# Kernel optimization log

Measured on AMD Instinct MI355X. Metric: run time of the kernel, lower is better.

Reference implementation:

```python
import jax, jax.numpy as jnp
import numpy as np

NEIGH = 0.4  # neighborhood_size from the module


def setup_inputs() -> dict:
    key = jax.random.key(0)
    ks = jax.random.split(key, 14)
    N, E, H, G, M = 1024, 64, 128, 8, 20
    OUT = 6 * M
    f32 = jnp.float32
    inp = {
        "xabs": jax.random.uniform(ks[0], (N, 2), f32),
        "i_h0": jax.random.normal(ks[1], (1, N, H), f32) * 0.1,
        "i_c0": jax.random.normal(ks[2], (1, N, H), f32) * 0.1,
        # I_Embedding: Linear(2, E)
        "W_emb": jax.random.normal(ks[3], (E, 2), f32) * 0.5,
        "b_emb": jax.random.normal(ks[4], (E,), f32) * 0.1,
        # embedding_social: Linear(G*G*H, E)
        "W_soc": jax.random.normal(ks[5], (E, G * G * H), f32) * (1.0 / np.sqrt(G * G * H)),
        "b_soc": jax.random.normal(ks[6], (E,), f32) * 0.1,
        # LSTM(2E -> H), torch gate order [i, f, g, o]
        "W_ih": jax.random.normal(ks[7], (4 * H, 2 * E), f32) * (1.0 / np.sqrt(2 * E)),
        "W_hh": jax.random.normal(ks[8], (4 * H, H), f32) * (1.0 / np.sqrt(H)),
        "b_ih": jax.random.normal(ks[9], (4 * H,), f32) * 0.05,
        "b_hh": jax.random.normal(ks[10], (4 * H,), f32) * 0.05,
        # I_Output: Linear(H, 6*M)
        "W_out": jax.random.normal(ks[11], (OUT, H), f32) * (1.0 / np.sqrt(H)),
        "b_out": jax.random.normal(ks[12], (OUT,), f32) * 0.05,
    }
    return inp


def _grid_mask(xabs, G):
    # Vectorized getGridMask: [N, N, G*G] one-hot bin membership.
    N = xabs.shape[0]
    # dx[n, m] = other_x - width_low(n); in-range iff 0 <= dx < NEIGH
    dx = xabs[None, :, 0] - (xabs[:, None, 0] - NEIGH / 2)
    dy = xabs[None, :, 1] - (xabs[:, None, 1] - NEIGH / 2)
    cell_x = jnp.floor(dx / NEIGH * G).astype(jnp.int32)
    cell_y = jnp.floor(dy / NEIGH * G).astype(jnp.int32)
    valid = (dx >= 0) & (dx < NEIGH) & (dy >= 0) & (dy < NEIGH)
    valid &= (cell_x >= 0) & (cell_x < G) & (cell_y >= 0) & (cell_y < G)
    valid &= ~jnp.eye(N, dtype=bool)  # skip self
    cell = jnp.where(valid, cell_x + cell_y * G, 0)
    mask = jax.nn.one_hot(cell, G * G, dtype=xabs.dtype)
    return mask * valid[:, :, None].astype(xabs.dtype)


def reference(xabs, i_h0, i_c0, W_emb, b_emb, W_soc, b_soc,
              W_ih, W_hh, b_ih, b_hh, W_out, b_out):
    N = xabs.shape[0]
    H = i_h0.shape[-1]
    G = int(np.sqrt(W_soc.shape[1] // H))
    M = W_out.shape[0] // 6

    # Input embedding
    emb_x = jax.nn.relu(xabs @ W_emb.T + b_emb)  # [N, E]

    # Social pooling: grid mask + scatter-reduce of hidden states
    h0 = i_h0[0]  # [N, H]
    mask = _grid_mask(xabs, G)  # [N, N, G*G]
    social = jnp.einsum('nmg,md->ngd', mask, h0)  # [N, G*G, H]
    social = social.reshape(N, G * G * H)
    pooling = jax.nn.relu(social @ W_soc.T + b_soc)  # [N, E]

    # Single LSTM step (seq len 1, 1 layer), torch gate order i,f,g,o
    lstm_in = jnp.concatenate([emb_x, pooling], axis=-1)  # [N, 2E]
    gates = lstm_in @ W_ih.T + b_ih + h0 @ W_hh.T + b_hh  # [N, 4H]
    i_g, f_g, g_g, o_g = jnp.split(gates, 4, axis=-1)
    c = jax.nn.sigmoid(f_g) * i_c0[0] + jax.nn.sigmoid(i_g) * jnp.tanh(g_g)
    h = jax.nn.sigmoid(o_g) * jnp.tanh(c)  # [N, H]

    final = h @ W_out.T + b_out  # [N, 6M]
    mu1, mu2, log_sigma1, log_sigma2, rho, pi_logits = jnp.split(final, 6, axis=1)
    return (mu1, mu2, log_sigma1, log_sigma2, rho, pi_logits)
```

## Files before the change

### kernel.cpp

```cpp
#include <hip/hip_runtime.h>
#include <hip/hip_bf16.h>
#include <math.h>

typedef __hip_bfloat16 bf16;
typedef short s8v __attribute__((ext_vector_type(8)));
typedef float f4v __attribute__((ext_vector_type(4)));

__device__ __forceinline__ float b2f(bf16 v) { return __bfloat162float(v); }

template <bool F32>
__device__ __forceinline__ float ld(const void* p, int i) {
  if (F32) return ((const float*)p)[i];
  return b2f(((const bf16*)p)[i]);
}

template <bool F32>
__device__ __forceinline__ s8v ldfrag(const void* p, size_t i) {
  if (F32) {
    const float* f = (const float*)p + i;
    float4 u = *reinterpret_cast<const float4*>(f);
    float4 v = *reinterpret_cast<const float4*>(f + 4);
    s8v r;
    bf16 t;
    t = __float2bfloat16(u.x); r[0] = *(short*)&t;
    t = __float2bfloat16(u.y); r[1] = *(short*)&t;
    t = __float2bfloat16(u.z); r[2] = *(short*)&t;
    t = __float2bfloat16(u.w); r[3] = *(short*)&t;
    t = __float2bfloat16(v.x); r[4] = *(short*)&t;
    t = __float2bfloat16(v.y); r[5] = *(short*)&t;
    t = __float2bfloat16(v.z); r[6] = *(short*)&t;
    t = __float2bfloat16(v.w); r[7] = *(short*)&t;
    return r;
  }
  return *reinterpret_cast<const s8v*>((const bf16*)p + i);
}

__device__ __forceinline__ float sigm(float x) {
  return 0.5f * (1.0f + tanhf(0.5f * x));
}

__device__ __forceinline__ bool detect_f32(const void* xabs) {
  unsigned short v = ((const unsigned short*)xabs)[threadIdx.x & 63];
  int ex = (v >> 7) & 0xFF;
  return __ballot(ex >= 0x93) != 0ull;
}

template <bool F32>
__device__ __forceinline__ void cvt_f4(const void* src, bf16* __restrict__ dst,
                                       int i4) {
  if (F32) {
    float4 v = reinterpret_cast<const float4*>(src)[i4];
    bf16 t[4] = {__float2bfloat16(v.x), __float2bfloat16(v.y),
                 __float2bfloat16(v.z), __float2bfloat16(v.w)};
    reinterpret_cast<uint2*>(dst)[i4] = *reinterpret_cast<uint2*>(t);
  } else {
    reinterpret_cast<uint2*>(dst)[i4] = reinterpret_cast<const uint2*>(src)[i4];
  }
}

template <bool F32>
__device__ __forceinline__ void zgemm_body(const void* h0, const void* Wsoc,
                                           const void* Wih, const void* Whh,
                                           const void* Wout,
                                           bf16* __restrict__ Z, bf16* Wih_b,
                                           bf16* Whh_b, bf16* Wout_b) {
  const int t4 = blockIdx.x * 256 + threadIdx.x;
  if (t4 < 16384)
    cvt_f4<F32>(Wih, Wih_b, t4);
  else if (t4 < 32768)
    cvt_f4<F32>(Whh, Whh_b, t4 - 16384);
  else if (t4 < 36608)
    cvt_f4<F32>(Wout, Wout_b, t4 - 32768);

  const int wave = threadIdx.x >> 6, lane = threadIdx.x & 63;
  const int mt = blockIdx.x & 15;
  const int g  = (blockIdx.x >> 4) * 4 + wave;
  const int r16 = lane & 15, quad = lane >> 4;

  s8v afr[4][4];
#pragma unroll
  for (int ms = 0; ms < 4; ++ms)
#pragma unroll
    for (int kq = 0; kq < 4; ++kq)
      afr[ms][kq] = ldfrag<F32>(
          h0, (size_t)(mt * 64 + ms * 16 + r16) * 128 + kq * 32 + quad * 8);

  f4v acc[4][4];
#pragma unroll
  for (int ms = 0; ms < 4; ++ms)
#pragma unroll
    for (int t = 0; t < 4; ++t) acc[ms][t] = (f4v){0.f, 0.f, 0.f, 0.f};

#pragma unroll
  for (int t = 0; t < 4; ++t) {
#pragma unroll
    for (int kq = 0; kq < 4; ++kq) {
      s8v bfr = ldfrag<F32>(
          Wsoc, (size_t)(t * 16 + r16) * 8192 + g * 128 + kq * 32 + quad * 8);
#pragma unroll
      for (int ms = 0; ms < 4; ++ms)
        acc[ms][t] = __builtin_amdgcn_mfma_f32_16x16x32_bf16(afr[ms][kq], bfr,
                                                             acc[ms][t], 0, 0, 0);
    }
  }
#pragma unroll
  for (int ms = 0; ms < 4; ++ms)
#pragma unroll
    for (int t = 0; t < 4; ++t)
#pragma unroll
      for (int reg = 0; reg < 4; ++reg)
        Z[(size_t)(mt * 64 + ms * 16 + quad * 4 + reg) * 4096 + g * 64 +
          t * 16 + r16] = __float2bfloat16(acc[ms][t][reg]);
}

__global__ __launch_bounds__(256, 1) void k_zgemm(
    const void* h0, const void* Wsoc, const void* Wih, const void* Whh,
    const void* Wout, bf16* __restrict__ Z, bf16* Wih_b, bf16* Whh_b,
    bf16* Wout_b, const void* xabs) {
  if (detect_f32(xabs))
    zgemm_body<true>(h0, Wsoc, Wih, Whh, Wout, Z, Wih_b, Whh_b, Wout_b);
  else
    zgemm_body<false>(h0, Wsoc, Wih, Whh, Wout, Z, Wih_b, Whh_b, Wout_b);
}

#define XS 264
#define HS 136

template <bool F32>
__device__ __forceinline__ void fused_body(
    const void* xabs, const void* h0, const void* Wemb, const void* bemb,
    const void* bsoc, const bf16* __restrict__ Wih_b,
    const bf16* __restrict__ Whh_b, const void* bih, const void* bhh,
    const void* c0, const bf16* __restrict__ Wout_b, const void* bout,
    const bf16* __restrict__ Z, void* out, char* smem) {
  float* G   = (float*)smem;
  int* lists = (int*)smem;
  bf16* Xb   = (bf16*)(smem + 32768);
  bf16* Hb   = (bf16*)(smem + 32768 + 16 * XS * 2);
  const int tid = threadIdx.x;
  const int wave = tid >> 6, lane = tid & 63;
  const int r16 = lane & 15, quad = lane >> 4;

  for (int idx = 4 * XS + tid; idx < 16 * XS; idx += 256)
    Xb[idx] = __float2bfloat16(0.f);
  for (int idx = 4 * HS + tid; idx < 16 * HS; idx += 256)
    Hb[idx] = __float2bfloat16(0.f);

  const int n = blockIdx.x * 4 + wave;
  const float xn = ld<F32>(xabs, 2 * n);
  const float yn = ld<F32>(xabs, 2 * n + 1);
  const float tx = xn - 0.2f, ty = yn - 0.2f;
  int* mylist = lists + wave * 1024;
  int cnt = 0;
  for (int c = 0; c < 16; ++c) {
    const int m = c * 64 + lane;
    float dx = ld<F32>(xabs, 2 * m) - tx;
    float dy = ld<F32>(xabs, 2 * m + 1) - ty;
    int cx = (int)floorf(dx / 0.4f * 8.0f);
    int cy = (int)floorf(dy / 0.4f * 8.0f);
    bool valid = (dx >= 0.f) & (dx < 0.4f) & (dy >= 0.f) & (dy < 0.4f) &
                 (cx >= 0) & (cx < 8) & (cy >= 0) & (cy < 8) & (m != n);
    unsigned long long msk = __ballot(valid);
    if (valid) {
      int pos = cnt + __popcll(msk & ((1ull << lane) - 1ull));
      mylist[pos] = (m << 6) | (cx + cy * 8);
    }
    cnt += __popcll(msk);
  }

  float s[16];
#pragma unroll
  for (int u = 0; u < 16; ++u) s[u] = 0.f;
  int i = 0;
  for (; i + 16 <= cnt; i += 16) {
    int e[16];
#pragma unroll
    for (int u = 0; u < 16; ++u) e[u] = mylist[i + u];
#pragma unroll
    for (int u = 0; u < 16; ++u)
      s[u] += b2f(Z[(size_t)(e[u] >> 6) * 4096 + (e[u] & 63) * 64 + lane]);
  }
  for (; i + 4 <= cnt; i += 4) {
    int e[4];
#pragma unroll
    for (int u = 0; u < 4; ++u) e[u] = mylist[i + u];
#pragma unroll
    for (int u = 0; u < 4; ++u)
      s[u] += b2f(Z[(size_t)(e[u] >> 6) * 4096 + (e[u] & 63) * 64 + lane]);
  }
  for (; i < cnt; ++i) {
    int e0 = mylist[i];
    s[0] += b2f(Z[(size_t)(e0 >> 6) * 4096 + (e0 & 63) * 64 + lane]);
  }
#pragma unroll
  for (int u = 0; u < 8; ++u) s[u] += s[u + 8];
  float pool = ((s[0] + s[1]) + (s[2] + s[3])) + ((s[4] + s[5]) + (s[6] + s[7]));
  pool = fmaxf(pool + ld<F32>(bsoc, lane), 0.f);
  float emb = fmaxf(ld<F32>(Wemb, lane * 2) * xn +
                        ld<F32>(Wemb, lane * 2 + 1) * yn + ld<F32>(bemb, lane),
                    0.f);
  Xb[wave * XS + lane] = __float2bfloat16(emb);
  Xb[wave * XS + 64 + lane] = __float2bfloat16(pool);
  Xb[wave * XS + 128 + lane] = __float2bfloat16(ld<F32>(h0, n * 128 + lane));
  Xb[wave * XS + 192 + lane] =
      __float2bfloat16(ld<F32>(h0, n * 128 + 64 + lane));
  __syncthreads();

  s8v afr[8];
#pragma unroll
  for (int kq = 0; kq < 8; ++kq)
    afr[kq] = *reinterpret_cast<const s8v*>(&Xb[r16 * XS + kq * 32 + quad * 8]);
  const int j0w = wave * 128;
  f4v bacc[8];
#pragma unroll
  for (int jt = 0; jt < 8; ++jt) bacc[jt] = (f4v){0.f, 0.f, 0.f, 0.f};
#pragma unroll
  for (int jt = 0; jt < 8; ++jt) {
    int j = j0w + jt * 16 + r16;
#pragma unroll
    for (int kq = 0; kq < 4; ++kq) {
      s8v bfr = *reinterpret_cast<const s8v*>(
          &Wih_b[(size_t)j * 128 + kq * 32 + quad * 8]);
      bacc[jt] = __builtin_amdgcn_mfma_f32_16x16x32_bf16(afr[kq], bfr, bacc[jt],
                                                         0, 0, 0);
    }
#pragma unroll
    for (int kq = 0; kq < 4; ++kq) {
      s8v bfr = *reinterpret_cast<const s8v*>(
          &Whh_b[(size_t)j * 128 + kq * 32 + quad * 8]);
      bacc[jt] = __builtin_amdgcn_mfma_f32_16x16x32_bf16(afr[kq + 4], bfr,
                                                         bacc[jt], 0, 0, 0);
    }
  }
#pragma unroll
  for (int jt = 0; jt < 8; ++jt) {
    int j = j0w + jt * 16 + r16;
    float bias = ld<F32>(bih, j) + ld<F32>(bhh, j);
#pragma unroll
    for (int reg = 0; reg < 4; ++reg)
      G[(quad * 4 + reg) * 512 + j] = bacc[jt][reg] + bias;
  }
  __syncthreads();

  for (int idx = tid; idx < 512; idx += 256) {
    int m = idx >> 7, tt = idx & 127;
    float ig = G[m * 512 + tt], fg = G[m * 512 + 128 + tt];
    float gg = G[m * 512 + 256 + tt], og = G[m * 512 + 384 + tt];
    float c = sigm(fg) * ld<F32>(c0, (blockIdx.x * 4 + m) * 128 + tt) +
              sigm(ig) * tanhf(gg);
    Hb[m * HS + tt] = __float2bfloat16(sigm(og) * tanhf(c));
  }
  __syncthreads();

  s8v hfr[4];
#pragma unroll
  for (int kq = 0; kq < 4; ++kq)
    hfr[kq] = *reinterpret_cast<const s8v*>(&Hb[r16 * HS + kq * 32 + quad * 8]);
#pragma unroll
  for (int jt2 = 0; jt2 < 2; ++jt2) {
    int j = wave * 32 + jt2 * 16 + r16;
    int jj = j < 120 ? j : 119;
    f4v oacc = (f4v){0.f, 0.f, 0.f, 0.f};
#pragma unroll
    for (int kq = 0; kq < 4; ++kq) {
      s8v bfr = *reinterpret_cast<const s8v*>(
          &Wout_b[(size_t)jj * 128 + kq * 32 + quad * 8]);
      oacc = __builtin_amdgcn_mfma_f32_16x16x32_bf16(hfr[kq], bfr, oacc, 0, 0, 0);
    }
    if (j < 120 && quad == 0) {
      float bo = ld<F32>(bout, j);
      int kk = j / 20, mm = j % 20;
#pragma unroll
      for (int reg = 0; reg < 4; ++reg) {
        int oi = kk * 20480 + (blockIdx.x * 4 + reg) * 20 + mm;
        float val = oacc[reg] + bo;
        if (F32) ((float*)out)[oi] = val;
        else     ((bf16*)out)[oi] = __float2bfloat16(val);
      }
    }
  }
}

__global__ __launch_bounds__(256, 1) void k_fused(
    const void* xabs, const void* h0, const void* Wemb, const void* bemb,
    const void* bsoc, const bf16* Wih_b, const bf16* Whh_b, const void* bih,
    const void* bhh, const void* c0, const bf16* Wout_b, const void* bout,
    const bf16* __restrict__ Z, void* out) {
  __shared__ __align__(16) char smem[32768 + 16 * XS * 2 + 16 * HS * 2];
  if (detect_f32(xabs))
    fused_body<true>(xabs, h0, Wemb, bemb, bsoc, Wih_b, Whh_b, bih, bhh, c0,
                     Wout_b, bout, Z, out, smem);
  else
    fused_body<false>(xabs, h0, Wemb, bemb, bsoc, Wih_b, Whh_b, bih, bhh, c0,
                      Wout_b, bout, Z, out, smem);
}

extern "C" void kernel_launch(void* const* d_in, const int* in_sizes, int n_in,
                              void* d_out, int out_size, void* d_ws, size_t ws_size,
                              hipStream_t stream) {
  const void* xabs = d_in[0];
  const void* h0   = d_in[1];
  const void* c0   = d_in[2];
  const void* Wemb = d_in[3];
  const void* bemb = d_in[4];
  const void* Wsoc = d_in[5];
  const void* bsoc = d_in[6];
  const void* Wih  = d_in[7];
  const void* Whh  = d_in[8];
  const void* bih  = d_in[9];
  const void* bhh  = d_in[10];
  const void* Wout = d_in[11];
  const void* bout = d_in[12];

  bf16* Z      = (bf16*)d_ws;
  bf16* Wih_b  = Z + (size_t)1024 * 4096;
  bf16* Whh_b  = Wih_b + (size_t)512 * 128;
  bf16* Wout_b = Whh_b + (size_t)512 * 128;

  k_zgemm<<<dim3(256), dim3(256), 0, stream>>>(h0, Wsoc, Wih, Whh, Wout, Z,
                                               Wih_b, Whh_b, Wout_b, xabs);
  k_fused<<<dim3(256), dim3(256), 0, stream>>>(xabs, h0, Wemb, bemb, bsoc,
                                               Wih_b, Whh_b, bih, bhh, c0,
                                               Wout_b, bout, Z, d_out);
}
```

Measured before the change: 122.0 us.

## Merge GEMM and fused LSTM kernels into one cooperative kernel with grid sync

Replaces the two back-to-back launches with a single cooperative kernel. A grid-wide barrier separates the Z projection GEMM from the neighbor gather. The neighbor-list build, input embedding and h0 staging now run before the barrier, so they overlap with the GEMM phase. This removes one launch and the inter-kernel gap, but adds the cost of a cooperative launch and a grid sync, and needs all 256 blocks to be co-resident.

```diff
diff --git a/kernel.cpp b/kernel.cpp
--- a/kernel.cpp
+++ b/kernel.cpp
@@ -1,6 +1,9 @@
 #include <hip/hip_runtime.h>
+#include <hip/hip_cooperative_groups.h>
 #include <hip/hip_bf16.h>
 #include <math.h>
+
+namespace cg = cooperative_groups;
 
 typedef __hip_bfloat16 bf16;
 typedef short s8v __attribute__((ext_vector_type(8)));
@@ -58,81 +61,16 @@
   }
 }
 
-template <bool F32>
-__device__ __forceinline__ void zgemm_body(const void* h0, const void* Wsoc,
-                                           const void* Wih, const void* Whh,
-                                           const void* Wout,
-                                           bf16* __restrict__ Z, bf16* Wih_b,
-                                           bf16* Whh_b, bf16* Wout_b) {
-  const int t4 = blockIdx.x * 256 + threadIdx.x;
-  if (t4 < 16384)
-    cvt_f4<F32>(Wih, Wih_b, t4);
-  else if (t4 < 32768)
-    cvt_f4<F32>(Whh, Whh_b, t4 - 16384);
-  else if (t4 < 36608)
-    cvt_f4<F32>(Wout, Wout_b, t4 - 32768);
-
-  const int wave = threadIdx.x >> 6, lane = threadIdx.x & 63;
-  const int mt = blockIdx.x & 15;
-  const int g  = (blockIdx.x >> 4) * 4 + wave;
-  const int r16 = lane & 15, quad = lane >> 4;
-
-  s8v afr[4][4];
-#pragma unroll
-  for (int ms = 0; ms < 4; ++ms)
-#pragma unroll
-    for (int kq = 0; kq < 4; ++kq)
-      afr[ms][kq] = ldfrag<F32>(
-          h0, (size_t)(mt * 64 + ms * 16 + r16) * 128 + kq * 32 + quad * 8);
-
-  f4v acc[4][4];
-#pragma unroll
-  for (int ms = 0; ms < 4; ++ms)
-#pragma unroll
-    for (int t = 0; t < 4; ++t) acc[ms][t] = (f4v){0.f, 0.f, 0.f, 0.f};
-
-#pragma unroll
-  for (int t = 0; t < 4; ++t) {
-#pragma unroll
-    for (int kq = 0; kq < 4; ++kq) {
-      s8v bfr = ldfrag<F32>(
-          Wsoc, (size_t)(t * 16 + r16) * 8192 + g * 128 + kq * 32 + quad * 8);
-#pragma unroll
-      for (int ms = 0; ms < 4; ++ms)
-        acc[ms][t] = __builtin_amdgcn_mfma_f32_16x16x32_bf16(afr[ms][kq], bfr,
-                                                             acc[ms][t], 0, 0, 0);
-    }
-  }
-#pragma unroll
-  for (int ms = 0; ms < 4; ++ms)
-#pragma unroll
-    for (int t = 0; t < 4; ++t)
-#pragma unroll
-      for (int reg = 0; reg < 4; ++reg)
-        Z[(size_t)(mt * 64 + ms * 16 + quad * 4 + reg) * 4096 + g * 64 +
-          t * 16 + r16] = __float2bfloat16(acc[ms][t][reg]);
-}
-
-__global__ __launch_bounds__(256, 1) void k_zgemm(
-    const void* h0, const void* Wsoc, const void* Wih, const void* Whh,
-    const void* Wout, bf16* __restrict__ Z, bf16* Wih_b, bf16* Whh_b,
-    bf16* Wout_b, const void* xabs) {
-  if (detect_f32(xabs))
-    zgemm_body<true>(h0, Wsoc, Wih, Whh, Wout, Z, Wih_b, Whh_b, Wout_b);
-  else
-    zgemm_body<false>(h0, Wsoc, Wih, Whh, Wout, Z, Wih_b, Whh_b, Wout_b);
-}
-
 #define XS 264
 #define HS 136
 
 template <bool F32>
-__device__ __forceinline__ void fused_body(
+__device__ __forceinline__ void run_all(
     const void* xabs, const void* h0, const void* Wemb, const void* bemb,
-    const void* bsoc, const bf16* __restrict__ Wih_b,
-    const bf16* __restrict__ Whh_b, const void* bih, const void* bhh,
-    const void* c0, const bf16* __restrict__ Wout_b, const void* bout,
-    const bf16* __restrict__ Z, void* out, char* smem) {
+    const void* Wsoc, const void* bsoc, const void* Wih, const void* Whh,
+    const void* bih, const void* bhh, const void* c0, const void* Wout,
+    const void* bout, bf16* __restrict__ Z, bf16* Wih_b, bf16* Whh_b,
+    bf16* Wout_b, void* out, char* smem, const cg::grid_group& grid) {
   float* G   = (float*)smem;
   int* lists = (int*)smem;
   bf16* Xb   = (bf16*)(smem + 32768);
@@ -140,13 +78,27 @@
   const int tid = threadIdx.x;
   const int wave = tid >> 6, lane = tid & 63;
   const int r16 = lane & 15, quad = lane >> 4;
-
-  for (int idx = 4 * XS + tid; idx < 16 * XS; idx += 256)
-    Xb[idx] = __float2bfloat16(0.f);
-  for (int idx = 4 * HS + tid; idx < 16 * HS; idx += 256)
-    Hb[idx] = __float2bfloat16(0.f);
-
-  const int n = blockIdx.x * 4 + wave;
+  const int bx = blockIdx.x;
+
+  const int t4 = bx * 256 + tid;
+  if (t4 < 16384)
+    cvt_f4<F32>(Wih, Wih_b, t4);
+  else if (t4 < 32768)
+    cvt_f4<F32>(Whh, Whh_b, t4 - 16384);
+  else if (t4 < 36608)
+    cvt_f4<F32>(Wout, Wout_b, t4 - 32768);
+
+  const int mt = bx & 15;
+  const int g  = (bx >> 4) * 4 + wave;
+  s8v afr[4][4];
+#pragma unroll
+  for (int ms = 0; ms < 4; ++ms)
+#pragma unroll
+    for (int kq = 0; kq < 4; ++kq)
+      afr[ms][kq] = ldfrag<F32>(
+          h0, (size_t)(mt * 64 + ms * 16 + r16) * 128 + kq * 32 + quad * 8);
+
+  const int n = bx * 4 + wave;
   const float xn = ld<F32>(xabs, 2 * n);
   const float yn = ld<F32>(xabs, 2 * n + 1);
   const float tx = xn - 0.2f, ty = yn - 0.2f;
@@ -168,6 +120,46 @@
     cnt += __popcll(msk);
   }
 
+  f4v acc[4][4];
+#pragma unroll
+  for (int ms = 0; ms < 4; ++ms)
+#pragma unroll
+    for (int t = 0; t < 4; ++t) acc[ms][t] = (f4v){0.f, 0.f, 0.f, 0.f};
+#pragma unroll
+  for (int t = 0; t < 4; ++t) {
+#pragma unroll
+    for (int kq = 0; kq < 4; ++kq) {
+      s8v bfr = ldfrag<F32>(
+          Wsoc, (size_t)(t * 16 + r16) * 8192 + g * 128 + kq * 32 + quad * 8);
+#pragma unroll
+      for (int ms = 0; ms < 4; ++ms)
+        acc[ms][t] = __builtin_amdgcn_mfma_f32_16x16x32_bf16(afr[ms][kq], bfr,
+                                                             acc[ms][t], 0, 0, 0);
+    }
+  }
+#pragma unroll
+  for (int ms = 0; ms < 4; ++ms)
+#pragma unroll
+    for (int t = 0; t < 4; ++t)
+#pragma unroll
+      for (int reg = 0; reg < 4; ++reg)
+        Z[(size_t)(mt * 64 + ms * 16 + quad * 4 + reg) * 4096 + g * 64 +
+          t * 16 + r16] = __float2bfloat16(acc[ms][t][reg]);
+
+  for (int idx = 4 * XS + tid; idx < 16 * XS; idx += 256)
+    Xb[idx] = __float2bfloat16(0.f);
+  for (int idx = 4 * HS + tid; idx < 16 * HS; idx += 256)
+    Hb[idx] = __float2bfloat16(0.f);
+  float emb = fmaxf(ld<F32>(Wemb, lane * 2) * xn +
+                        ld<F32>(Wemb, lane * 2 + 1) * yn + ld<F32>(bemb, lane),
+                    0.f);
+  Xb[wave * XS + lane] = __float2bfloat16(emb);
+  Xb[wave * XS + 128 + lane] = __float2bfloat16(ld<F32>(h0, n * 128 + lane));
+  Xb[wave * XS + 192 + lane] =
+      __float2bfloat16(ld<F32>(h0, n * 128 + 64 + lane));
+
+  grid.sync();
+
   float s[16];
 #pragma unroll
   for (int u = 0; u < 16; ++u) s[u] = 0.f;
@@ -196,20 +188,13 @@
   for (int u = 0; u < 8; ++u) s[u] += s[u + 8];
   float pool = ((s[0] + s[1]) + (s[2] + s[3])) + ((s[4] + s[5]) + (s[6] + s[7]));
   pool = fmaxf(pool + ld<F32>(bsoc, lane), 0.f);
-  float emb = fmaxf(ld<F32>(Wemb, lane * 2) * xn +
-                        ld<F32>(Wemb, lane * 2 + 1) * yn + ld<F32>(bemb, lane),
-                    0.f);
-  Xb[wave * XS + lane] = __float2bfloat16(emb);
   Xb[wave * XS + 64 + lane] = __float2bfloat16(pool);
-  Xb[wave * XS + 128 + lane] = __float2bfloat16(ld<F32>(h0, n * 128 + lane));
-  Xb[wave * XS + 192 + lane] =
-      __float2bfloat16(ld<F32>(h0, n * 128 + 64 + lane));
   __syncthreads();
 
-  s8v afr[8];
+  s8v xfr[8];
 #pragma unroll
   for (int kq = 0; kq < 8; ++kq)
-    afr[kq] = *reinterpret_cast<const s8v*>(&Xb[r16 * XS + kq * 32 + quad * 8]);
+    xfr[kq] = *reinterpret_cast<const s8v*>(&Xb[r16 * XS + kq * 32 + quad * 8]);
   const int j0w = wave * 128;
   f4v bacc[8];
 #pragma unroll
@@ -221,14 +206,14 @@
     for (int kq = 0; kq < 4; ++kq) {
       s8v bfr = *reinterpret_cast<const s8v*>(
           &Wih_b[(size_t)j * 128 + kq * 32 + quad * 8]);
-      bacc[jt] = __builtin_amdgcn_mfma_f32_16x16x32_bf16(afr[kq], bfr, bacc[jt],
+      bacc[jt] = __builtin_amdgcn_mfma_f32_16x16x32_bf16(xfr[kq], bfr, bacc[jt],
                                                          0, 0, 0);
     }
 #pragma unroll
     for (int kq = 0; kq < 4; ++kq) {
       s8v bfr = *reinterpret_cast<const s8v*>(
           &Whh_b[(size_t)j * 128 + kq * 32 + quad * 8]);
-      bacc[jt] = __builtin_amdgcn_mfma_f32_16x16x32_bf16(afr[kq + 4], bfr,
+      bacc[jt] = __builtin_amdgcn_mfma_f32_16x16x32_bf16(xfr[kq + 4], bfr,
                                                          bacc[jt], 0, 0, 0);
     }
   }
@@ -246,7 +231,7 @@
     int m = idx >> 7, tt = idx & 127;
     float ig = G[m * 512 + tt], fg = G[m * 512 + 128 + tt];
     float gg = G[m * 512 + 256 + tt], og = G[m * 512 + 384 + tt];
-    float c = sigm(fg) * ld<F32>(c0, (blockIdx.x * 4 + m) * 128 + tt) +
+    float c = sigm(fg) * ld<F32>(c0, (bx * 4 + m) * 128 + tt) +
               sigm(ig) * tanhf(gg);
     Hb[m * HS + tt] = __float2bfloat16(sigm(og) * tanhf(c));
   }
@@ -272,7 +257,7 @@
       int kk = j / 20, mm = j % 20;
 #pragma unroll
       for (int reg = 0; reg < 4; ++reg) {
-        int oi = kk * 20480 + (blockIdx.x * 4 + reg) * 20 + mm;
+        int oi = kk * 20480 + (bx * 4 + reg) * 20 + mm;
         float val = oacc[reg] + bo;
         if (F32) ((float*)out)[oi] = val;
         else     ((bf16*)out)[oi] = __float2bfloat16(val);
@@ -281,18 +266,20 @@
   }
 }
 
-__global__ __launch_bounds__(256, 1) void k_fused(
+__global__ __launch_bounds__(256, 1) void k_all(
     const void* xabs, const void* h0, const void* Wemb, const void* bemb,
-    const void* bsoc, const bf16* Wih_b, const bf16* Whh_b, const void* bih,
-    const void* bhh, const void* c0, const bf16* Wout_b, const void* bout,
-    const bf16* __restrict__ Z, void* out) {
+    const void* Wsoc, const void* bsoc, const void* Wih, const void* Whh,
+    const void* bih, const void* bhh, const void* c0, const void* Wout,
+    const void* bout, bf16* Z, bf16* Wih_b, bf16* Whh_b, bf16* Wout_b,
+    void* out) {
   __shared__ __align__(16) char smem[32768 + 16 * XS * 2 + 16 * HS * 2];
+  cg::grid_group grid = cg::this_grid();
   if (detect_f32(xabs))
-    fused_body<true>(xabs, h0, Wemb, bemb, bsoc, Wih_b, Whh_b, bih, bhh, c0,
-                     Wout_b, bout, Z, out, smem);
+    run_all<true>(xabs, h0, Wemb, bemb, Wsoc, bsoc, Wih, Whh, bih, bhh, c0,
+                  Wout, bout, Z, Wih_b, Whh_b, Wout_b, out, smem, grid);
   else
-    fused_body<false>(xabs, h0, Wemb, bemb, bsoc, Wih_b, Whh_b, bih, bhh, c0,
-                      Wout_b, bout, Z, out, smem);
+    run_all<false>(xabs, h0, Wemb, bemb, Wsoc, bsoc, Wih, Whh, bih, bhh, c0,
+                   Wout, bout, Z, Wih_b, Whh_b, Wout_b, out, smem, grid);
 }
 
 extern "C" void kernel_launch(void* const* d_in, const int* in_sizes, int n_in,
@@ -316,10 +303,11 @@
   bf16* Wih_b  = Z + (size_t)1024 * 4096;
   bf16* Whh_b  = Wih_b + (size_t)512 * 128;
   bf16* Wout_b = Whh_b + (size_t)512 * 128;
-
-  k_zgemm<<<dim3(256), dim3(256), 0, stream>>>(h0, Wsoc, Wih, Whh, Wout, Z,
-                                               Wih_b, Whh_b, Wout_b, xabs);
-  k_fused<<<dim3(256), dim3(256), 0, stream>>>(xabs, h0, Wemb, bemb, bsoc,
-                                               Wih_b, Whh_b, bih, bhh, c0,
-                                               Wout_b, bout, Z, d_out);
-}
+  void* outp   = d_out;
+
+  void* args[] = {&xabs, &h0,  &Wemb, &bemb, &Wsoc,  &bsoc,  &Wih,
+                  &Whh,  &bih, &bhh,  &c0,   &Wout,  &bout,  &Z,
+                  &Wih_b, &Whh_b, &Wout_b, &outp};
+  hipLaunchCooperativeKernel((void*)k_all, dim3(256), dim3(256), args, 0,
+                             stream);
+}
```

After: 174.4 us. 42.9% more time.
